# Optimization experiments

Measured on AMD Instinct MI355X. Metric: run time of the kernel, lower is better.

The kernel has to match this reference:

```python
import jax, jax.numpy as jnp
import numpy as np
import math

B, T, C = 2, 2048, 2048
H, KV, HD = 16, 4, 128  # num_heads, num_kv_heads, head_dim
REP = H // KV


def _rope_tables(T, hd, base=10000.0):
    inv_freq = 1.0 / (base ** (np.arange(0, hd, 2, dtype=np.float32) / hd))  # [hd/2]
    t = np.arange(T, dtype=np.float32)
    freqs = np.outer(t, inv_freq)                 # [T, hd/2]
    emb = np.concatenate([freqs, freqs], axis=-1)  # [T, hd]
    return jnp.asarray(np.cos(emb)), jnp.asarray(np.sin(emb))


def setup_inputs() -> dict:
    key = jax.random.key(0)
    ks = jax.random.split(key, 5)
    cos, sin = _rope_tables(T, HD)
    std = 0.02
    return {
        "x": jax.random.normal(ks[0], (B, T, C), dtype=jnp.float32),
        "cos": cos,
        "sin": sin,
        "Wq": jax.random.normal(ks[1], (C, H * HD), dtype=jnp.float32) * std,
        "Wk": jax.random.normal(ks[2], (C, KV * HD), dtype=jnp.float32) * std,
        "Wv": jax.random.normal(ks[3], (C, KV * HD), dtype=jnp.float32) * std,
        "Wo": jax.random.normal(ks[4], (H * HD, C), dtype=jnp.float32) * std,
    }


def _rotate_half(t):
    h = t.shape[-1] // 2
    return jnp.concatenate([-t[..., h:], t[..., :h]], axis=-1)


def reference(x, cos, sin, Wq, Wk, Wv, Wo):
    Bx, Tx, Cx = x.shape
    q = (x @ Wq).reshape(Bx, Tx, H, HD).transpose(0, 2, 1, 3)   # [B,H,T,hd]
    k = (x @ Wk).reshape(Bx, Tx, KV, HD).transpose(0, 2, 1, 3)  # [B,KV,T,hd]
    v = (x @ Wv).reshape(Bx, Tx, KV, HD).transpose(0, 2, 1, 3)
    c = cos[None, None]  # [1,1,T,hd]
    s = sin[None, None]
    q = q * c + _rotate_half(q) * s
    k = k * c + _rotate_half(k) * s
    # repeat_kv: expand KV heads to H heads (interleave within groups)
    k = jnp.repeat(k, REP, axis=1)  # [B,H,T,hd]
    v = jnp.repeat(v, REP, axis=1)
    scores = jnp.einsum("bhqd,bhkd->bhqk", q, k) / math.sqrt(HD)
    causal = jnp.triu(jnp.full((Tx, Tx), float("-inf"), dtype=scores.dtype), k=1)
    scores = jax.nn.softmax(scores + causal[None, None], axis=-1)
    out = jnp.einsum("bhqk,bhkd->bhqd", scores, v)  # [B,H,T,hd]
    out = out.transpose(0, 2, 1, 3).reshape(Bx, Tx, H * HD)
    return out @ Wo
```

## Files before the change

### kernel.cpp

```cpp
#include <hip/hip_runtime.h>
#include <hip/hip_bf16.h>
#include <math.h>

typedef __bf16 bf16_t;
typedef __bf16 bf16x8 __attribute__((ext_vector_type(8)));
typedef float f32x4 __attribute__((ext_vector_type(4)));

constexpr int Bc = 2, Tc = 2048, Cdim = 2048, Hc = 16, KVc = 4, HDc = 128;
constexpr int Mc = Bc * Tc;
constexpr int Nqkv = 3072;

typedef const __attribute__((address_space(1))) void* as1_cptr;
typedef __attribute__((address_space(3))) void* as3_ptr;

__device__ __forceinline__ void gload_lds16(const bf16_t* g, bf16_t* l) {
  __builtin_amdgcn_global_load_lds((as1_cptr)(const void*)g, (as3_ptr)(void*)l, 16, 0, 0);
}

__device__ __forceinline__ unsigned int cvt_pk_bf16(float lo, float hi) {
  unsigned int r;
  asm("v_cvt_pk_bf16_f32 %0, %1, %2" : "=v"(r) : "v"(lo), "v"(hi));
  return r;
}
__device__ __forceinline__ void perm32swap(unsigned int& a, unsigned int& b) {
  asm("v_permlane32_swap_b32 %0, %1" : "+v"(a), "+v"(b));
}
__device__ __forceinline__ void perm16swap(unsigned int& a, unsigned int& b) {
  asm("v_permlane16_swap_b32 %0, %1" : "+v"(a), "+v"(b));
}
__device__ __forceinline__ float fast_exp2(float x) {
  float r;
  asm("v_exp_f32 %0, %1" : "=v"(r) : "v"(x));
  return r;
}

__global__ void k_prep(const float* __restrict__ x, bf16_t* __restrict__ xb,
                       const float* __restrict__ Wq, const float* __restrict__ Wk,
                       const float* __restrict__ Wv, const float* __restrict__ Wo,
                       bf16_t* __restrict__ Wqt, bf16_t* __restrict__ Wkt,
                       bf16_t* __restrict__ Wvt, bf16_t* __restrict__ Wot) {
  __shared__ bf16_t tile[64][73];
  int bid = blockIdx.x;
  if (bid < 4096) {
    int i = (bid * 256 + threadIdx.x) * 8;
    float4 a = *(const float4*)(x + i);
    float4 b = *(const float4*)(x + i + 4);
    bf16x8 v;
    v[0] = (bf16_t)a.x; v[1] = (bf16_t)a.y; v[2] = (bf16_t)a.z; v[3] = (bf16_t)a.w;
    v[4] = (bf16_t)b.x; v[5] = (bf16_t)b.y; v[6] = (bf16_t)b.z; v[7] = (bf16_t)b.w;
    *(bf16x8*)(xb + i) = v;
    return;
  }
  bid -= 4096;
  const float* W; bf16_t* Wt; int K, N, k0, n0;
  if (bid < 1024)      { W = Wq; Wt = Wqt; K = 2048; N = 2048; k0 = (bid >> 5) * 64; n0 = (bid & 31) * 64; }
  else if (bid < 1280) { bid -= 1024; W = Wk; Wt = Wkt; K = 2048; N = 512; k0 = (bid >> 3) * 64; n0 = (bid & 7) * 64; }
  else if (bid < 1536) { bid -= 1280; W = Wv; Wt = Wvt; K = 2048; N = 512; k0 = (bid >> 3) * 64; n0 = (bid & 7) * 64; }
  else                 { bid -= 1536; W = Wo; Wt = Wot; K = 2048; N = 2048; k0 = (bid >> 5) * 64; n0 = (bid & 31) * 64; }
  const int t = threadIdx.x;
#pragma unroll
  for (int i = 0; i < 4; ++i) {
    int idx = t + i * 256;
    int r = idx >> 4;
    int c4 = (idx & 15) * 4;
    float4 v = *(const float4*)(W + (size_t)(k0 + r) * N + n0 + c4);
    tile[r][c4 + 0] = (bf16_t)v.x; tile[r][c4 + 1] = (bf16_t)v.y;
    tile[r][c4 + 2] = (bf16_t)v.z; tile[r][c4 + 3] = (bf16_t)v.w;
  }
  __syncthreads();
#pragma unroll
  for (int i = 0; i < 4; ++i) {
    int idx = t + i * 256;
    int n = idx >> 4;
    int kc = (idx & 15) * 4;
    alignas(8) bf16_t o[4];
#pragma unroll
    for (int j = 0; j < 4; ++j) o[j] = tile[kc + j][n];
    *(uint2*)(Wt + (size_t)(n0 + n) * K + k0 + kc) = *(uint2*)o;
  }
}

__global__ __launch_bounds__(256, 2) void k_gemm_bt(
    const bf16_t* __restrict__ A, const bf16_t* __restrict__ Bt,
    float* __restrict__ Cout, int M, int N, int K) {
  __shared__ alignas(16) bf16_t Ash[128 * 64];
  __shared__ alignas(16) bf16_t Bsh[128 * 64];
  const int tid = threadIdx.x;
  const int wave = tid >> 6, lane = tid & 63;
  const int col = lane & 15, quad = lane >> 4;
  const int gx = gridDim.x;
  const int nwg = gx * gridDim.y;
  int wg = blockIdx.y * gx + blockIdx.x;
  if ((nwg & 7) == 0) wg = (wg & 7) * (nwg >> 3) + (wg >> 3);
  const int m0 = (wg / gx) * 128, n0 = (wg % gx) * 128;
  const int wr = wave >> 1, wc = wave & 1;

  f32x4 acc[4][4];
#pragma unroll
  for (int i = 0; i < 4; ++i)
#pragma unroll
    for (int j = 0; j < 4; ++j) acc[i][j] = f32x4{0.f, 0.f, 0.f, 0.f};

  const int lrow = lane >> 3;
  const int lkc8 = (lane & 7) ^ lrow;

  for (int k0 = 0; k0 < K; k0 += 64) {
    __syncthreads();
#pragma unroll
    for (int i = 0; i < 4; ++i) {
      const int rb = wave * 32 + i * 8;
      gload_lds16(A + (size_t)(m0 + rb + lrow) * K + k0 + lkc8 * 8, Ash + rb * 64);
      gload_lds16(Bt + (size_t)(n0 + rb + lrow) * K + k0 + lkc8 * 8, Bsh + rb * 64);
    }
    __syncthreads();
#pragma unroll
    for (int kc = 0; kc < 2; ++kc) {
      bf16x8 af[4], bfr[4];
#pragma unroll
      for (int mt = 0; mt < 4; ++mt) {
        const int m = wr * 64 + mt * 16 + col;
        const int slot = (kc * 4 + quad) ^ (m & 7);
        af[mt] = *(const bf16x8*)(Ash + m * 64 + slot * 8);
      }
#pragma unroll
      for (int nt = 0; nt < 4; ++nt) {
        const int n = wc * 64 + nt * 16 + col;
        const int slot = (kc * 4 + quad) ^ (n & 7);
        bfr[nt] = *(const bf16x8*)(Bsh + n * 64 + slot * 8);
      }
#pragma unroll
      for (int mt = 0; mt < 4; ++mt)
#pragma unroll
        for (int nt = 0; nt < 4; ++nt)
          acc[mt][nt] = __builtin_amdgcn_mfma_f32_16x16x32_bf16(
              af[mt], bfr[nt], acc[mt][nt], 0, 0, 0);
    }
  }
#pragma unroll
  for (int mt = 0; mt < 4; ++mt)
#pragma unroll
    for (int i = 0; i < 4; ++i) {
      const int row = m0 + wr * 64 + mt * 16 + quad * 4 + i;
#pragma unroll
      for (int nt = 0; nt < 4; ++nt)
        Cout[(size_t)row * N + n0 + wc * 64 + nt * 16 + col] = acc[mt][nt][i];
    }
}

__global__ __launch_bounds__(256, 3) void k_gemm_qkv(
    const bf16_t* __restrict__ A, const bf16_t* __restrict__ Bt,
    const float* __restrict__ cs, const float* __restrict__ sn,
    bf16_t* __restrict__ Qp, bf16_t* __restrict__ Kp, bf16_t* __restrict__ Vt) {
  constexpr int K = Cdim;
  __shared__ alignas(16) bf16_t Ash[128 * 64];
  __shared__ alignas(16) bf16_t Bsh[128 * 64];
  const int tid = threadIdx.x;
  const int wave = tid >> 6, lane = tid & 63;
  const int col = lane & 15, quad = lane >> 4;
  const int gx = gridDim.x;
  const int nwg = gx * gridDim.y;
  int wg = blockIdx.y * gx + blockIdx.x;
  wg = (wg & 7) * (nwg >> 3) + (wg >> 3);
  const int m0 = (wg / gx) * 128;
  const int bxi = wg % gx;
  const int n0 = bxi * 128;

  f32x4 acc[2][8];
#pragma unroll
  for (int i = 0; i < 2; ++i)
#pragma unroll
    for (int j = 0; j < 8; ++j) acc[i][j] = f32x4{0.f, 0.f, 0.f, 0.f};

  const int lrow = lane >> 3;
  const int lkc8 = (lane & 7) ^ lrow;

  for (int k0 = 0; k0 < K; k0 += 64) {
    __syncthreads();
#pragma unroll
    for (int i = 0; i < 4; ++i) {
      const int rb = wave * 32 + i * 8;
      gload_lds16(A + (size_t)(m0 + rb + lrow) * K + k0 + lkc8 * 8, Ash + rb * 64);
      gload_lds16(Bt + (size_t)(n0 + rb + lrow) * K + k0 + lkc8 * 8, Bsh + rb * 64);
    }
    __syncthreads();
#pragma unroll
    for (int kc = 0; kc < 2; ++kc) {
      bf16x8 af[2], bfr[8];
#pragma unroll
      for (int mt = 0; mt < 2; ++mt) {
        const int m = wave * 32 + mt * 16 + col;
        const int slot = (kc * 4 + quad) ^ (m & 7);
        af[mt] = *(const bf16x8*)(Ash + m * 64 + slot * 8);
      }
#pragma unroll
      for (int nt = 0; nt < 8; ++nt) {
        const int n = nt * 16 + col;
        const int slot = (kc * 4 + quad) ^ (n & 7);
        bfr[nt] = *(const bf16x8*)(Bsh + n * 64 + slot * 8);
      }
#pragma unroll
      for (int mt = 0; mt < 2; ++mt)
#pragma unroll
        for (int nt = 0; nt < 8; ++nt)
          acc[mt][nt] = __builtin_amdgcn_mfma_f32_16x16x32_bf16(
              af[mt], bfr[nt], acc[mt][nt], 0, 0, 0);
    }
  }

  const int bx = bxi;
  if (bx < 20) {
    const bool isQ = bx < 16;
#pragma unroll
    for (int mt = 0; mt < 2; ++mt)
#pragma unroll
      for (int i = 0; i < 4; ++i) {
        const int row = m0 + wave * 32 + mt * 16 + quad * 4 + i;
        const int b = row >> 11, t = row & (Tc - 1);
        bf16_t* op = isQ ? Qp + ((size_t)(b * Hc + bx) * Tc + t) * HDc
                         : Kp + ((size_t)(b * KVc + (bx - 16)) * Tc + t) * HDc;
        const float* cr = cs + t * HDc;
        const float* sr = sn + t * HDc;
#pragma unroll
        for (int nt = 0; nt < 4; ++nt) {
          const int d = nt * 16 + col;
          const float c = cr[d], s = sr[d];
          const float x0 = acc[mt][nt][i], x1 = acc[mt][nt + 4][i];
          op[d]      = (bf16_t)(x0 * c - x1 * s);
          op[d + 64] = (bf16_t)(x1 * c + x0 * s);
        }
      }
  } else {
    const int kv = bx - 20;
#pragma unroll
    for (int mt = 0; mt < 2; ++mt) {
      const int row0 = m0 + wave * 32 + mt * 16 + quad * 4;
      const int b = row0 >> 11, t0 = row0 & (Tc - 1);
#pragma unroll
      for (int nt = 0; nt < 8; ++nt) {
        const int d = nt * 16 + col;
        alignas(8) bf16_t o[4];
#pragma unroll
        for (int i = 0; i < 4; ++i) o[i] = (bf16_t)acc[mt][nt][i];
        *(uint2*)(Vt + ((size_t)(b * KVc + kv) * HDc + d) * Tc + t0) = *(uint2*)o;
      }
    }
  }
}

__global__ __launch_bounds__(512, 2) void k_attn(
    const bf16_t* __restrict__ Qp, const bf16_t* __restrict__ Kp,
    const bf16_t* __restrict__ Vt, bf16_t* __restrict__ Oout) {
  constexpr float sc2 = 0.08838834764831845f * 1.4426950408889634f;
  __shared__ alignas(16) bf16_t Ksh[2][2][64 * 128];
  __shared__ alignas(16) bf16_t Vsh[2][2][128 * 64];
  __shared__ float lex[4][64][2];

  const int wg = blockIdx.x;
  const int g = wg & 7, k = wg >> 3;
  const int kvh = g & 3, b = g >> 2;
  const int h = kvh * 4 + (k >> 3);
  const int i2 = k & 7;

  const int tid = threadIdx.x, wave = tid >> 6, lane = tid & 63;
  const int wq = wave & 3, wk = wave >> 2;
  const int col = lane & 15, quad = lane >> 4;

  const bf16_t* Kb = Kp + (size_t)(b * KVc + kvh) * Tc * HDc;
  const bf16_t* Vb = Vt + (size_t)(b * KVc + kvh) * HDc * Tc;
  const bf16_t* Qbh = Qp + (size_t)(b * Hc + h) * Tc * HDc;

  const int st_kr = lane >> 4, st_kc8 = lane & 15;
  const int st_vr = lane >> 3, st_vc8 = lane & 7;

  const int qt0 = 15 - i2, qt1 = i2;
  const int PT0 = qt0 + 1;
  const int PTOT = 17;

  int q0 = qt0 * 128 + wq * 32;

  bf16x8 qfA[4], qfB[4];
  {
    const bf16_t* qa = Qbh + (size_t)(q0 + col) * HDc;
    const bf16_t* qb = Qbh + (size_t)(q0 + 16 + col) * HDc;
#pragma unroll
    for (int kc = 0; kc < 4; ++kc) {
      bf16x8 ra = *(const bf16x8*)(qa + kc * 32 + quad * 8);
      bf16x8 rb = *(const bf16x8*)(qb + kc * 32 + quad * 8);
#pragma unroll
      for (int e = 0; e < 8; ++e) {
        qfA[kc][e] = (bf16_t)((float)ra[e] * sc2);
        qfB[kc][e] = (bf16_t)((float)rb[e] * sc2);
      }
    }
  }

  f32x4 o_accA[8], o_accB[8];
#pragma unroll
  for (int nb = 0; nb < 8; ++nb) {
    o_accA[nb] = f32x4{0.f, 0.f, 0.f, 0.f};
    o_accB[nb] = f32x4{0.f, 0.f, 0.f, 0.f};
  }
  float l_iA = 0.f, l_iB = 0.f;

  auto stage = [&](int bufi, int kbase) {
    bf16_t* Kd = &Ksh[bufi][wk][0];
    bf16_t* Vd = &Vsh[bufi][wk][0];
    const int kb = kbase + wk * 64;
#pragma unroll
    for (int i = 0; i < 4; ++i) {
      const int rb = wq * 16 + i * 4;
      const int r = rb + st_kr;
      const int kc8 = st_kc8 ^ (r & 7);
      gload_lds16(Kb + (size_t)(kb + r) * HDc + kc8 * 8, Kd + rb * 128);
      const int db = wq * 32 + i * 8;
      const int d = db + st_vr;
      const int tc8 = st_vc8 ^ (d & 7);
      gload_lds16(Vb + (size_t)d * Tc + kb + tc8 * 8, Vd + db * 64);
    }
  };

  auto combine = [&](int bufc) {
    asm volatile("s_barrier" ::: "memory");
    float* xo = (wq < 2) ? (float*)(&Ksh[bufc][0][0]) + wq * 4096
                         : (float*)(&Vsh[bufc][0][0]) + (wq - 2) * 4096;
    if (wk) {
#pragma unroll
      for (int nb = 0; nb < 8; ++nb) {
        *(f32x4*)(xo + nb * 256 + lane * 4) = o_accA[nb];
        *(f32x4*)(xo + (8 + nb) * 256 + lane * 4) = o_accB[nb];
      }
      lex[wq][lane][0] = l_iA;
      lex[wq][lane][1] = l_iB;
    }
    asm volatile("s_waitcnt lgkmcnt(0)" ::: "memory");
    asm volatile("s_barrier" ::: "memory");
    if (!wk) {
#pragma unroll
      for (int nb = 0; nb < 8; ++nb) {
        o_accA[nb] += *(const f32x4*)(xo + nb * 256 + lane * 4);
        o_accB[nb] += *(const f32x4*)(xo + (8 + nb) * 256 + lane * 4);
      }
      float lA = l_iA + lex[wq][lane][0];
      float lB = l_iB + lex[wq][lane][1];
#pragma unroll
      for (int gg = 0; gg < 2; ++gg) {
        float rs = gg ? lB : lA;
        rs += __shfl_xor(rs, 16);
        rs += __shfl_xor(rs, 32);
        const float inv = 1.0f / rs;
        const f32x4* oa = gg ? o_accB : o_accA;
        const int qbase = q0 + gg * 16;
#pragma unroll
        for (int i = 0; i < 4; ++i) {
          const float iq = __shfl(inv, quad * 4 + i);
          const int qrow = qbase + quad * 4 + i;
          bf16_t* op = Oout + ((size_t)(b * Tc) + qrow) * (Hc * HDc) + h * HDc;
#pragma unroll
          for (int nb = 0; nb < 8; ++nb) op[nb * 16 + col] = (bf16_t)(oa[nb][i] * iq);
        }
      }
    }
  };

  stage(0, 0);

#pragma unroll 1
  for (int t = 0; t < PTOT; ++t) {
    const int cur = t & 1;
    const bool diag = (t == PT0 - 1) || (t == PTOT - 1);
    const int tn = (t < PT0) ? t : t - PT0;
    const int kb = tn * 128 + wk * 64;
    asm volatile("s_barrier" ::: "memory");
    {
      const int jn = (t + 1 < PTOT) ? (t + 1) : (PTOT - 1);
      const int tnn = (jn < PT0) ? jn : jn - PT0;
      stage(cur ^ 1, tnn * 128);
    }
    asm volatile("s_waitcnt vmcnt(8)" ::: "memory");
    asm volatile("s_barrier" ::: "memory");

    const bf16_t* Kc = &Ksh[cur][wk][0];
    const bf16_t* Vc = &Vsh[cur][wk][0];

    f32x4 stA[4], stB[4];
#pragma unroll
    for (int tb = 0; tb < 4; ++tb) {
      stA[tb] = f32x4{0.f, 0.f, 0.f, 0.f};
      stB[tb] = f32x4{0.f, 0.f, 0.f, 0.f};
    }
    __builtin_amdgcn_s_setprio(1);
#pragma unroll
    for (int kc = 0; kc < 4; ++kc)
#pragma unroll
      for (int tb = 0; tb < 4; ++tb) {
        const int r = tb * 16 + col;
        const int slot = (kc * 4 + quad) ^ (r & 7);
        bf16x8 kf = *(const bf16x8*)(Kc + r * 128 + slot * 8);
        stA[tb] = __builtin_amdgcn_mfma_f32_16x16x32_bf16(kf, qfA[kc], stA[tb], 0, 0, 0);
        stB[tb] = __builtin_amdgcn_mfma_f32_16x16x32_bf16(kf, qfB[kc], stB[tb], 0, 0, 0);
      }
    __builtin_amdgcn_s_setprio(0);

    unsigned int pwA[4][2], pwB[4][2];
    const int qrA = q0 + col, qrB = q0 + 16 + col;
#pragma unroll
    for (int tb = 0; tb < 4; ++tb) {
      const int kvb = kb + tb * 16 + quad * 4;
      float a0 = fast_exp2(stA[tb][0]), a1 = fast_exp2(stA[tb][1]);
      float a2 = fast_exp2(stA[tb][2]), a3 = fast_exp2(stA[tb][3]);
      float b0 = fast_exp2(stB[tb][0]), b1 = fast_exp2(stB[tb][1]);
      float b2 = fast_exp2(stB[tb][2]), b3 = fast_exp2(stB[tb][3]);
      if (diag) {
        a0 = (kvb + 0 > qrA) ? 0.f : a0;
        a1 = (kvb + 1 > qrA) ? 0.f : a1;
        a2 = (kvb + 2 > qrA) ? 0.f : a2;
        a3 = (kvb + 3 > qrA) ? 0.f : a3;
        b0 = (kvb + 0 > qrB) ? 0.f : b0;
        b1 = (kvb + 1 > qrB) ? 0.f : b1;
        b2 = (kvb + 2 > qrB) ? 0.f : b2;
        b3 = (kvb + 3 > qrB) ? 0.f : b3;
      }
      l_iA += (a0 + a1) + (a2 + a3);
      l_iB += (b0 + b1) + (b2 + b3);
      pwA[tb][0] = cvt_pk_bf16(a0, a1);
      pwA[tb][1] = cvt_pk_bf16(a2, a3);
      pwB[tb][0] = cvt_pk_bf16(b0, b1);
      pwB[tb][1] = cvt_pk_bf16(b2, b3);
    }

#pragma unroll
    for (int kc = 0; kc < 2; ++kc) {
      unsigned int a0 = pwA[2 * kc][0], c0 = pwA[2 * kc + 1][0];
      unsigned int a1 = pwA[2 * kc][1], c1 = pwA[2 * kc + 1][1];
      perm32swap(a0, c0); perm32swap(a1, c1);
      perm16swap(a0, c0); perm16swap(a1, c1);
      union { unsigned int w[4]; bf16x8 v; } uA;
      uA.w[0] = a0; uA.w[1] = a1; uA.w[2] = c0; uA.w[3] = c1;
      unsigned int d0 = pwB[2 * kc][0], e0 = pwB[2 * kc + 1][0];
      unsigned int d1 = pwB[2 * kc][1], e1 = pwB[2 * kc + 1][1];
      perm32swap(d0, e0); perm32swap(d1, e1);
      perm16swap(d0, e0); perm16swap(d1, e1);
      union { unsigned int w[4]; bf16x8 v; } uB;
      uB.w[0] = d0; uB.w[1] = d1; uB.w[2] = e0; uB.w[3] = e1;
      const bf16x8 pfA = uA.v, pfB = uB.v;
      __builtin_amdgcn_s_setprio(1);
#pragma unroll
      for (int nb = 0; nb < 8; ++nb) {
        const int d = nb * 16 + col;
        const int vslot = (kc * 4 + quad) ^ (d & 7);
        bf16x8 vf = *(const bf16x8*)(Vc + d * 64 + vslot * 8);
        o_accA[nb] = __builtin_amdgcn_mfma_f32_16x16x32_bf16(pfA, vf, o_accA[nb], 0, 0, 0);
        o_accB[nb] = __builtin_amdgcn_mfma_f32_16x16x32_bf16(pfB, vf, o_accB[nb], 0, 0, 0);
      }
      __builtin_amdgcn_s_setprio(0);
    }

    if (t == PT0 - 1) {
      combine(cur);
      l_iA = 0.f; l_iB = 0.f;
#pragma unroll
      for (int nb = 0; nb < 8; ++nb) {
        o_accA[nb] = f32x4{0.f, 0.f, 0.f, 0.f};
        o_accB[nb] = f32x4{0.f, 0.f, 0.f, 0.f};
      }
      q0 = qt1 * 128 + wq * 32;
      const bf16_t* qa = Qbh + (size_t)(q0 + col) * HDc;
      const bf16_t* qb = Qbh + (size_t)(q0 + 16 + col) * HDc;
#pragma unroll
      for (int kc = 0; kc < 4; ++kc) {
        bf16x8 ra = *(const bf16x8*)(qa + kc * 32 + quad * 8);
        bf16x8 rb = *(const bf16x8*)(qb + kc * 32 + quad * 8);
#pragma unroll
        for (int e = 0; e < 8; ++e) {
          qfA[kc][e] = (bf16_t)((float)ra[e] * sc2);
          qfB[kc][e] = (bf16_t)((float)rb[e] * sc2);
        }
      }
    }
  }

  combine((PTOT - 1) & 1);
}

extern "C" void kernel_launch(void* const* d_in, const int* in_sizes, int n_in,
                              void* d_out, int out_size, void* d_ws, size_t ws_size,
                              hipStream_t stream) {
  (void)in_sizes; (void)n_in; (void)out_size; (void)ws_size;
  const float* x    = (const float*)d_in[0];
  const float* cosT = (const float*)d_in[1];
  const float* sinT = (const float*)d_in[2];
  const float* Wq   = (const float*)d_in[3];
  const float* Wk   = (const float*)d_in[4];
  const float* Wv   = (const float*)d_in[5];
  const float* Wo   = (const float*)d_in[6];
  float* out = (float*)d_out;

  char* ws = (char*)d_ws;
  size_t off = 0;
  auto take = [&](size_t bytes) { char* p = ws + off; off += (bytes + 255) & ~(size_t)255; return p; };

  bf16_t* xb    = (bf16_t*)take((size_t)Mc * Cdim * 2);
  bf16_t* Wqkvt = (bf16_t*)take((size_t)Nqkv * Cdim * 2);
  bf16_t* Wot   = (bf16_t*)take((size_t)Cdim * (Hc * HDc) * 2);
  bf16_t* Qp    = (bf16_t*)take((size_t)Mc * (Hc * HDc) * 2);
  bf16_t* Kp    = (bf16_t*)take((size_t)Mc * (KVc * HDc) * 2);
  bf16_t* Vt    = (bf16_t*)take((size_t)Mc * (KVc * HDc) * 2);
  bf16_t* Wqt = Wqkvt;
  bf16_t* Wkt = Wqkvt + (size_t)2048 * Cdim;
  bf16_t* Wvt = Wqkvt + (size_t)2560 * Cdim;
  bf16_t* attn = xb;

  k_prep<<<dim3(4096 + 1024 + 256 + 256 + 1024), dim3(256), 0, stream>>>(
      x, xb, Wq, Wk, Wv, Wo, Wqt, Wkt, Wvt, Wot);
  k_gemm_qkv<<<dim3(Nqkv / 128, Mc / 128), dim3(256), 0, stream>>>(
      xb, Wqkvt, cosT, sinT, Qp, Kp, Vt);
  k_attn<<<dim3(256), dim3(512), 0, stream>>>(Qp, Kp, Vt, attn);
  k_gemm_bt<<<dim3(Cdim / 128, Mc / 128), dim3(256), 0, stream>>>(
      attn, Wot, out, Mc, Cdim, Hc * HDc);
}
```

Baseline: 268.1 us.

## Software-pipeline attention loop: overlap QK of next tile with PV of previous

```diff
diff --git a/kernel.cpp b/kernel.cpp
--- a/kernel.cpp
+++ b/kernel.cpp
@@ -256,10 +256,10 @@
   __shared__ float lex[4][64][2];
 
   const int wg = blockIdx.x;
-  const int g = wg & 7, k = wg >> 3;
+  const int g = wg & 7, kslot = wg >> 3;
   const int kvh = g & 3, b = g >> 2;
-  const int h = kvh * 4 + (k >> 3);
-  const int i2 = k & 7;
+  const int h = kvh * 4 + (kslot >> 3);
+  const int i2 = kslot & 7;
 
   const int tid = threadIdx.x, wave = tid >> 6, lane = tid & 63;
   const int wq = wave & 3, wk = wave >> 2;
@@ -274,44 +274,60 @@
 
   const int qt0 = 15 - i2, qt1 = i2;
   const int PT0 = qt0 + 1;
-  const int PTOT = 17;
-
-  int q0 = qt0 * 128 + wq * 32;
-
-  bf16x8 qfA[4], qfB[4];
+
+  const int q0p0 = qt0 * 128 + wq * 32;
+  const int q0p1 = qt1 * 128 + wq * 32;
+  int q0 = q0p0;
+
+  bf16x8 qA0[4], qB0[4], qA1[4], qB1[4];
   {
-    const bf16_t* qa = Qbh + (size_t)(q0 + col) * HDc;
-    const bf16_t* qb = Qbh + (size_t)(q0 + 16 + col) * HDc;
+    const bf16_t* a0 = Qbh + (size_t)(q0p0 + col) * HDc;
+    const bf16_t* b0 = Qbh + (size_t)(q0p0 + 16 + col) * HDc;
+    const bf16_t* a1 = Qbh + (size_t)(q0p1 + col) * HDc;
+    const bf16_t* b1 = Qbh + (size_t)(q0p1 + 16 + col) * HDc;
 #pragma unroll
     for (int kc = 0; kc < 4; ++kc) {
-      bf16x8 ra = *(const bf16x8*)(qa + kc * 32 + quad * 8);
-      bf16x8 rb = *(const bf16x8*)(qb + kc * 32 + quad * 8);
+      bf16x8 r0 = *(const bf16x8*)(a0 + kc * 32 + quad * 8);
+      bf16x8 r1 = *(const bf16x8*)(b0 + kc * 32 + quad * 8);
+      bf16x8 r2 = *(const bf16x8*)(a1 + kc * 32 + quad * 8);
+      bf16x8 r3 = *(const bf16x8*)(b1 + kc * 32 + quad * 8);
 #pragma unroll
       for (int e = 0; e < 8; ++e) {
-        qfA[kc][e] = (bf16_t)((float)ra[e] * sc2);
-        qfB[kc][e] = (bf16_t)((float)rb[e] * sc2);
-      }
-    }
-  }
-
-  f32x4 o_accA[8], o_accB[8];
+        qA0[kc][e] = (bf16_t)((float)r0[e] * sc2);
+        qB0[kc][e] = (bf16_t)((float)r1[e] * sc2);
+        qA1[kc][e] = (bf16_t)((float)r2[e] * sc2);
+        qB1[kc][e] = (bf16_t)((float)r3[e] * sc2);
+      }
+    }
+  }
+
+  f32x4 oA[8], oB[8];
 #pragma unroll
   for (int nb = 0; nb < 8; ++nb) {
-    o_accA[nb] = f32x4{0.f, 0.f, 0.f, 0.f};
-    o_accB[nb] = f32x4{0.f, 0.f, 0.f, 0.f};
-  }
-  float l_iA = 0.f, l_iB = 0.f;
-
-  auto stage = [&](int bufi, int kbase) {
-    bf16_t* Kd = &Ksh[bufi][wk][0];
-    bf16_t* Vd = &Vsh[bufi][wk][0];
-    const int kb = kbase + wk * 64;
+    oA[nb] = f32x4{0.f, 0.f, 0.f, 0.f};
+    oB[nb] = f32x4{0.f, 0.f, 0.f, 0.f};
+  }
+  float lA = 0.f, lB = 0.f;
+  unsigned int pwA[4][2], pwB[4][2];
+
+  auto kvb_of = [&](int t) { const int tn = (t < PT0) ? t : t - PT0; return tn * 128 + wk * 64; };
+
+  auto stageK = [&](int t) {
+    bf16_t* Kd = &Ksh[t & 1][wk][0];
+    const int kb = kvb_of(t);
 #pragma unroll
     for (int i = 0; i < 4; ++i) {
       const int rb = wq * 16 + i * 4;
       const int r = rb + st_kr;
       const int kc8 = st_kc8 ^ (r & 7);
       gload_lds16(Kb + (size_t)(kb + r) * HDc + kc8 * 8, Kd + rb * 128);
+    }
+  };
+  auto stageV = [&](int t) {
+    bf16_t* Vd = &Vsh[t & 1][wk][0];
+    const int kb = kvb_of(t);
+#pragma unroll
+    for (int i = 0; i < 4; ++i) {
       const int db = wq * 32 + i * 8;
       const int d = db + st_vr;
       const int tc8 = st_vc8 ^ (d & 7);
@@ -319,115 +335,21 @@
     }
   };
 
-  auto combine = [&](int bufc) {
-    asm volatile("s_barrier" ::: "memory");
-    float* xo = (wq < 2) ? (float*)(&Ksh[bufc][0][0]) + wq * 4096
-                         : (float*)(&Vsh[bufc][0][0]) + (wq - 2) * 4096;
-    if (wk) {
-#pragma unroll
-      for (int nb = 0; nb < 8; ++nb) {
-        *(f32x4*)(xo + nb * 256 + lane * 4) = o_accA[nb];
-        *(f32x4*)(xo + (8 + nb) * 256 + lane * 4) = o_accB[nb];
-      }
-      lex[wq][lane][0] = l_iA;
-      lex[wq][lane][1] = l_iB;
-    }
-    asm volatile("s_waitcnt lgkmcnt(0)" ::: "memory");
-    asm volatile("s_barrier" ::: "memory");
-    if (!wk) {
-#pragma unroll
-      for (int nb = 0; nb < 8; ++nb) {
-        o_accA[nb] += *(const f32x4*)(xo + nb * 256 + lane * 4);
-        o_accB[nb] += *(const f32x4*)(xo + (8 + nb) * 256 + lane * 4);
-      }
-      float lA = l_iA + lex[wq][lane][0];
-      float lB = l_iB + lex[wq][lane][1];
-#pragma unroll
-      for (int gg = 0; gg < 2; ++gg) {
-        float rs = gg ? lB : lA;
-        rs += __shfl_xor(rs, 16);
-        rs += __shfl_xor(rs, 32);
-        const float inv = 1.0f / rs;
-        const f32x4* oa = gg ? o_accB : o_accA;
-        const int qbase = q0 + gg * 16;
-#pragma unroll
-        for (int i = 0; i < 4; ++i) {
-          const float iq = __shfl(inv, quad * 4 + i);
-          const int qrow = qbase + quad * 4 + i;
-          bf16_t* op = Oout + ((size_t)(b * Tc) + qrow) * (Hc * HDc) + h * HDc;
-#pragma unroll
-          for (int nb = 0; nb < 8; ++nb) op[nb * 16 + col] = (bf16_t)(oa[nb][i] * iq);
-        }
-      }
-    }
+  auto qkc = [&](const bf16x8 (&qa)[4], const bf16x8 (&qb)[4],
+                 f32x4 (&sA)[4], f32x4 (&sB)[4], const bf16_t* Kc) {
+#pragma unroll
+    for (int kc = 0; kc < 4; ++kc)
+#pragma unroll
+      for (int tb = 0; tb < 4; ++tb) {
+        const int rr = tb * 16 + col;
+        const int slot = (kc * 4 + quad) ^ (rr & 7);
+        bf16x8 kf = *(const bf16x8*)(Kc + rr * 128 + slot * 8);
+        sA[tb] = __builtin_amdgcn_mfma_f32_16x16x32_bf16(kf, qa[kc], sA[tb], 0, 0, 0);
+        sB[tb] = __builtin_amdgcn_mfma_f32_16x16x32_bf16(kf, qb[kc], sB[tb], 0, 0, 0);
+      }
   };
 
-  stage(0, 0);
-
-#pragma unroll 1
-  for (int t = 0; t < PTOT; ++t) {
-    const int cur = t & 1;
-    const bool diag = (t == PT0 - 1) || (t == PTOT - 1);
-    const int tn = (t < PT0) ? t : t - PT0;
-    const int kb = tn * 128 + wk * 64;
-    asm volatile("s_barrier" ::: "memory");
-    {
-      const int jn = (t + 1 < PTOT) ? (t + 1) : (PTOT - 1);
-      const int tnn = (jn < PT0) ? jn : jn - PT0;
-      stage(cur ^ 1, tnn * 128);
-    }
-    asm volatile("s_waitcnt vmcnt(8)" ::: "memory");
-    asm volatile("s_barrier" ::: "memory");
-
-    const bf16_t* Kc = &Ksh[cur][wk][0];
-    const bf16_t* Vc = &Vsh[cur][wk][0];
-
-    f32x4 stA[4], stB[4];
-#pragma unroll
-    for (int tb = 0; tb < 4; ++tb) {
-      stA[tb] = f32x4{0.f, 0.f, 0.f, 0.f};
-      stB[tb] = f32x4{0.f, 0.f, 0.f, 0.f};
-    }
-    __builtin_amdgcn_s_setprio(1);
-#pragma unroll
-    for (int kc = 0; kc < 4; ++kc)
-#pragma unroll
-      for (int tb = 0; tb < 4; ++tb) {
-        const int r = tb * 16 + col;
-        const int slot = (kc * 4 + quad) ^ (r & 7);
-        bf16x8 kf = *(const bf16x8*)(Kc + r * 128 + slot * 8);
-        stA[tb] = __builtin_amdgcn_mfma_f32_16x16x32_bf16(kf, qfA[kc], stA[tb], 0, 0, 0);
-        stB[tb] = __builtin_amdgcn_mfma_f32_16x16x32_bf16(kf, qfB[kc], stB[tb], 0, 0, 0);
-      }
-    __builtin_amdgcn_s_setprio(0);
-
-    unsigned int pwA[4][2], pwB[4][2];
-    const int qrA = q0 + col, qrB = q0 + 16 + col;
-#pragma unroll
-    for (int tb = 0; tb < 4; ++tb) {
-      const int kvb = kb + tb * 16 + quad * 4;
-      float a0 = fast_exp2(stA[tb][0]), a1 = fast_exp2(stA[tb][1]);
-      float a2 = fast_exp2(stA[tb][2]), a3 = fast_exp2(stA[tb][3]);
-      float b0 = fast_exp2(stB[tb][0]), b1 = fast_exp2(stB[tb][1]);
-      float b2 = fast_exp2(stB[tb][2]), b3 = fast_exp2(stB[tb][3]);
-      if (diag) {
-        a0 = (kvb + 0 > qrA) ? 0.f : a0;
-        a1 = (kvb + 1 > qrA) ? 0.f : a1;
-        a2 = (kvb + 2 > qrA) ? 0.f : a2;
-        a3 = (kvb + 3 > qrA) ? 0.f : a3;
-        b0 = (kvb + 0 > qrB) ? 0.f : b0;
-        b1 = (kvb + 1 > qrB) ? 0.f : b1;
-        b2 = (kvb + 2 > qrB) ? 0.f : b2;
-        b3 = (kvb + 3 > qrB) ? 0.f : b3;
-      }
-      l_iA += (a0 + a1) + (a2 + a3);
-      l_iB += (b0 + b1) + (b2 + b3);
-      pwA[tb][0] = cvt_pk_bf16(a0, a1);
-      pwA[tb][1] = cvt_pk_bf16(a2, a3);
-      pwB[tb][0] = cvt_pk_bf16(b0, b1);
-      pwB[tb][1] = cvt_pk_bf16(b2, b3);
-    }
-
+  auto pvc = [&](const bf16_t* Vc) {
 #pragma unroll
     for (int kc = 0; kc < 2; ++kc) {
       unsigned int a0 = pwA[2 * kc][0], c0 = pwA[2 * kc + 1][0];
@@ -443,43 +365,137 @@
       union { unsigned int w[4]; bf16x8 v; } uB;
       uB.w[0] = d0; uB.w[1] = d1; uB.w[2] = e0; uB.w[3] = e1;
       const bf16x8 pfA = uA.v, pfB = uB.v;
-      __builtin_amdgcn_s_setprio(1);
 #pragma unroll
       for (int nb = 0; nb < 8; ++nb) {
         const int d = nb * 16 + col;
         const int vslot = (kc * 4 + quad) ^ (d & 7);
         bf16x8 vf = *(const bf16x8*)(Vc + d * 64 + vslot * 8);
-        o_accA[nb] = __builtin_amdgcn_mfma_f32_16x16x32_bf16(pfA, vf, o_accA[nb], 0, 0, 0);
-        o_accB[nb] = __builtin_amdgcn_mfma_f32_16x16x32_bf16(pfB, vf, o_accB[nb], 0, 0, 0);
-      }
-      __builtin_amdgcn_s_setprio(0);
-    }
-
-    if (t == PT0 - 1) {
-      combine(cur);
-      l_iA = 0.f; l_iB = 0.f;
+        oA[nb] = __builtin_amdgcn_mfma_f32_16x16x32_bf16(pfA, vf, oA[nb], 0, 0, 0);
+        oB[nb] = __builtin_amdgcn_mfma_f32_16x16x32_bf16(pfB, vf, oB[nb], 0, 0, 0);
+      }
+    }
+  };
+
+  auto expp = [&](const f32x4 (&sA)[4], const f32x4 (&sB)[4], int kb, bool diag) {
+    const int qrA = q0 + col, qrB = q0 + 16 + col;
+#pragma unroll
+    for (int tb = 0; tb < 4; ++tb) {
+      const int kvb = kb + tb * 16 + quad * 4;
+      float a0 = fast_exp2(sA[tb][0]), a1 = fast_exp2(sA[tb][1]);
+      float a2 = fast_exp2(sA[tb][2]), a3 = fast_exp2(sA[tb][3]);
+      float b0 = fast_exp2(sB[tb][0]), b1 = fast_exp2(sB[tb][1]);
+      float b2 = fast_exp2(sB[tb][2]), b3 = fast_exp2(sB[tb][3]);
+      if (diag) {
+        a0 = (kvb + 0 > qrA) ? 0.f : a0;
+        a1 = (kvb + 1 > qrA) ? 0.f : a1;
+        a2 = (kvb + 2 > qrA) ? 0.f : a2;
+        a3 = (kvb + 3 > qrA) ? 0.f : a3;
+        b0 = (kvb + 0 > qrB) ? 0.f : b0;
+        b1 = (kvb + 1 > qrB) ? 0.f : b1;
+        b2 = (kvb + 2 > qrB) ? 0.f : b2;
+        b3 = (kvb + 3 > qrB) ? 0.f : b3;
+      }
+      lA += (a0 + a1) + (a2 + a3);
+      lB += (b0 + b1) + (b2 + b3);
+      pwA[tb][0] = cvt_pk_bf16(a0, a1);
+      pwA[tb][1] = cvt_pk_bf16(a2, a3);
+      pwB[tb][0] = cvt_pk_bf16(b0, b1);
+      pwB[tb][1] = cvt_pk_bf16(b2, b3);
+    }
+  };
+
+  auto combine = [&](float* dead, int q0o) {
+    float* xo = dead + wq * 2048;
+    asm volatile("s_barrier" ::: "memory");
+    if (wk) {
+#pragma unroll
+      for (int nb = 0; nb < 8; ++nb) *(f32x4*)(xo + nb * 256 + lane * 4) = oA[nb];
+      lex[wq][lane][0] = lA;
+      lex[wq][lane][1] = lB;
+    }
+    asm volatile("s_waitcnt lgkmcnt(0)" ::: "memory");
+    asm volatile("s_barrier" ::: "memory");
+    if (!wk) {
+#pragma unroll
+      for (int nb = 0; nb < 8; ++nb) oA[nb] += *(const f32x4*)(xo + nb * 256 + lane * 4);
+    }
+    asm volatile("s_barrier" ::: "memory");
+    if (wk) {
+#pragma unroll
+      for (int nb = 0; nb < 8; ++nb) *(f32x4*)(xo + nb * 256 + lane * 4) = oB[nb];
+    }
+    asm volatile("s_waitcnt lgkmcnt(0)" ::: "memory");
+    asm volatile("s_barrier" ::: "memory");
+    if (!wk) {
+#pragma unroll
+      for (int nb = 0; nb < 8; ++nb) oB[nb] += *(const f32x4*)(xo + nb * 256 + lane * 4);
+      const float fA = lA + lex[wq][lane][0];
+      const float fB = lB + lex[wq][lane][1];
+#pragma unroll
+      for (int gg = 0; gg < 2; ++gg) {
+        float rs = gg ? fB : fA;
+        rs += __shfl_xor(rs, 16);
+        rs += __shfl_xor(rs, 32);
+        const float inv = 1.0f / rs;
+        const f32x4* oa = gg ? oB : oA;
+        const int qbase = q0o + gg * 16;
+#pragma unroll
+        for (int i = 0; i < 4; ++i) {
+          const float iq = __shfl(inv, quad * 4 + i);
+          const int qrow = qbase + quad * 4 + i;
+          bf16_t* op = Oout + ((size_t)(b * Tc) + qrow) * (Hc * HDc) + h * HDc;
+#pragma unroll
+          for (int nb = 0; nb < 8; ++nb) op[nb * 16 + col] = (bf16_t)(oa[nb][i] * iq);
+        }
+      }
+    }
+  };
+
+  stageK(0); stageV(0);
+
+#pragma unroll 1
+  for (int r = 0; r <= 16; ++r) {
+    asm volatile("s_barrier" ::: "memory");
+    stageK(r < 16 ? r + 1 : 16);
+    stageV(r);
+    asm volatile("s_waitcnt vmcnt(8)" ::: "memory");
+    asm volatile("s_barrier" ::: "memory");
+
+    f32x4 stA[4], stB[4];
+#pragma unroll
+    for (int tb = 0; tb < 4; ++tb) {
+      stA[tb] = f32x4{0.f, 0.f, 0.f, 0.f};
+      stB[tb] = f32x4{0.f, 0.f, 0.f, 0.f};
+    }
+    const bf16_t* Kc = &Ksh[r & 1][wk][0];
+    __builtin_amdgcn_s_setprio(1);
+    if (r < PT0) qkc(qA0, qB0, stA, stB, Kc);
+    else         qkc(qA1, qB1, stA, stB, Kc);
+    if (r >= 1)  pvc(&Vsh[(r - 1) & 1][wk][0]);
+    __builtin_amdgcn_s_setprio(0);
+
+    if (r == PT0) {
+      combine((float*)&Vsh[(PT0 - 1) & 1][0][0], q0);
 #pragma unroll
       for (int nb = 0; nb < 8; ++nb) {
-        o_accA[nb] = f32x4{0.f, 0.f, 0.f, 0.f};
-        o_accB[nb] = f32x4{0.f, 0.f, 0.f, 0.f};
-      }
-      q0 = qt1 * 128 + wq * 32;
-      const bf16_t* qa = Qbh + (size_t)(q0 + col) * HDc;
-      const bf16_t* qb = Qbh + (size_t)(q0 + 16 + col) * HDc;
-#pragma unroll
-      for (int kc = 0; kc < 4; ++kc) {
-        bf16x8 ra = *(const bf16x8*)(qa + kc * 32 + quad * 8);
-        bf16x8 rb = *(const bf16x8*)(qb + kc * 32 + quad * 8);
-#pragma unroll
-        for (int e = 0; e < 8; ++e) {
-          qfA[kc][e] = (bf16_t)((float)ra[e] * sc2);
-          qfB[kc][e] = (bf16_t)((float)rb[e] * sc2);
-        }
-      }
-    }
-  }
-
-  combine((PTOT - 1) & 1);
+        oA[nb] = f32x4{0.f, 0.f, 0.f, 0.f};
+        oB[nb] = f32x4{0.f, 0.f, 0.f, 0.f};
+      }
+      lA = 0.f; lB = 0.f;
+      q0 = q0p1;
+    }
+
+    const bool diag = (r == PT0 - 1) || (r == 16);
+    expp(stA, stB, kvb_of(r), diag);
+  }
+
+  asm volatile("s_barrier" ::: "memory");
+  asm volatile("s_waitcnt vmcnt(0)" ::: "memory");
+  asm volatile("s_barrier" ::: "memory");
+  __builtin_amdgcn_s_setprio(1);
+  pvc(&Vsh[0][wk][0]);
+  __builtin_amdgcn_s_setprio(0);
+  combine((float*)&Vsh[1][0][0], q0);
 }
 
 extern "C" void kernel_launch(void* const* d_in, const int* in_sizes, int n_in,
```

After: 289.9 us. +8.1%, slower.
